# Optimization experiments

Hardware: AMD Instinct MI355X
Metric: run time of the kernel (lower is better)

The kernel has to match this reference:

```python
import jax, jax.numpy as jnp
import numpy as np

N_NODES = 1500
N_EDGES = 12000
IN_FEAT = 512
HIDDEN = 64
OUT_FEAT = 32
HEADS = 8
NEG_SLOPE = 0.2  # DGL GATConv default leaky_relu slope


def setup_inputs() -> dict:
    key = jax.random.key(0)
    ks = jax.random.split(key, 16)

    def xav(k, shape, fan_in):
        return jax.random.normal(k, shape, jnp.float32) * (1.0 / np.sqrt(fan_in))

    return {
        "node": jax.random.normal(ks[0], (N_NODES, IN_FEAT), jnp.float32),
        "src": jax.random.randint(ks[1], (N_EDGES,), 0, N_NODES, jnp.int32),
        "dst": jax.random.randint(ks[2], (N_EDGES,), 0, N_NODES, jnp.int32),
        "W1": xav(ks[3], (IN_FEAT, HEADS * HIDDEN), IN_FEAT),
        "al1": xav(ks[4], (HEADS, HIDDEN), HIDDEN),
        "ar1": xav(ks[5], (HEADS, HIDDEN), HIDDEN),
        "b1": jnp.zeros((HEADS, HIDDEN), jnp.float32),
        "W2": xav(ks[6], (HIDDEN, HEADS * HIDDEN), HIDDEN),
        "al2": xav(ks[7], (HEADS, HIDDEN), HIDDEN),
        "ar2": xav(ks[8], (HEADS, HIDDEN), HIDDEN),
        "b2": jnp.zeros((HEADS, HIDDEN), jnp.float32),
        "W3": xav(ks[9], (HIDDEN, HEADS * OUT_FEAT), HIDDEN),
        "al3": xav(ks[10], (HEADS, OUT_FEAT), OUT_FEAT),
        "ar3": xav(ks[11], (HEADS, OUT_FEAT), OUT_FEAT),
        "b3": jnp.zeros((HEADS, OUT_FEAT), jnp.float32),
    }


def gat_layer(h, W, al, ar, b, src, dst, n_nodes):
    """DGL GATConv semantics: h has shape [N, *prefix, F_in]; output [N, *prefix, H, F_out]."""
    H, Fo = al.shape
    feat = (h @ W).reshape(h.shape[:-1] + (H, Fo))          # [N, *P, H, Fo]
    el = (feat * al).sum(-1)                                 # [N, *P, H]
    er = (feat * ar).sum(-1)                                 # [N, *P, H]
    e = jax.nn.leaky_relu(el[src] + er[dst], NEG_SLOPE)      # [E, *P, H]
    # numerically stable edge softmax over incoming edges of each dst node
    emax = jax.lax.stop_gradient(jax.ops.segment_max(e, dst, num_segments=n_nodes))
    ex = jnp.exp(e - emax[dst])
    den = jax.ops.segment_sum(ex, dst, num_segments=n_nodes)
    a = ex / den[dst]                                        # [E, *P, H]
    msg = a[..., None] * feat[src]                           # [E, *P, H, Fo]
    return jax.ops.segment_sum(msg, dst, num_segments=n_nodes) + b


def reference(node, src, dst, W1, al1, ar1, b1, W2, al2, ar2, b2, W3, al3, ar3, b3):
    n = node.shape[0]
    h = gat_layer(node, W1, al1, ar1, b1, src, dst, n)       # [N, 8, 64]
    h = jax.nn.gelu(h, approximate=False)
    h = gat_layer(h, W2, al2, ar2, b2, src, dst, n)          # [N, 8, 8, 64]
    h = jax.nn.gelu(h, approximate=False)
    return gat_layer(h, W3, al3, ar3, b3, src, dst, n)       # [N, 8, 8, 8, 32]
```

## Files before the change

### kernel.cpp

```cpp
#include <hip/hip_runtime.h>
#include <math.h>

#define N_NODES 1500
#define N_EDGES 12000
#define IN_FEAT 512
#define HIDDEN 64
#define OUT_FEAT 32
#define HEADS 8

typedef short bf16x8 __attribute__((ext_vector_type(8)));
typedef float f32x4 __attribute__((ext_vector_type(4)));

__device__ __forceinline__ unsigned short f2bf(float f) {
    unsigned u = __float_as_uint(f);
    u += 0x7fff + ((u >> 16) & 1);
    return (unsigned short)(u >> 16);
}
__device__ __forceinline__ float bf2f(unsigned short b) {
    return __uint_as_float(((unsigned)b) << 16);
}
__device__ __forceinline__ unsigned packbf(float a) {
    unsigned short hi = f2bf(a);
    unsigned short lo = f2bf(a - bf2f(hi));
    return (unsigned)hi | ((unsigned)lo << 16);
}
__device__ __forceinline__ float rdlanef(float v, int c) {
    return __uint_as_float(__builtin_amdgcn_readlane(__float_as_uint(v), c));
}


__global__ void prep_kernel(const float* __restrict__ W2, const float* __restrict__ al2,
                            const float* __restrict__ ar2,
                            const float* __restrict__ W3, const float* __restrict__ al3,
                            const float* __restrict__ ar3,
                            float* __restrict__ aleff2, float* __restrict__ areff2,
                            float* __restrict__ aleff3, float* __restrict__ areff3,
                            float* __restrict__ W4t2,
                            unsigned* __restrict__ wfhi, unsigned* __restrict__ wflo,
                            int* __restrict__ counts, int* __restrict__ cursor) {
    int i = blockIdx.x * blockDim.x + threadIdx.x;
    if (i < 1536) {
        if (i < N_NODES + 1) counts[i] = 0;
        return;
    }
    i -= 1536;
    if (i < 1536) {
        if (i < N_NODES) cursor[i] = 0;
        return;
    }
    i -= 1536;
    if (i < 1024) {
        int lr = i >> 9; i &= 511;
        int h = i >> 6, k = i & 63;
        const float* a = lr ? ar2 : al2;
        float s = 0.f;
        for (int f = 0; f < 64; ++f)
            s = fmaf(W2[(size_t)k * 512 + h * 64 + f], a[h * 64 + f], s);
        (lr ? areff2 : aleff2)[h * 64 + k] = s;
        return;
    }
    i -= 1024;
    if (i < 1024) {
        int lr = i >> 9; i &= 511;
        int h = i >> 6, k = i & 63;
        const float* a = lr ? ar3 : al3;
        float s = 0.f;
        for (int f = 0; f < 32; ++f)
            s = fmaf(W3[(size_t)k * 256 + h * 32 + f], a[h * 32 + f], s);
        (lr ? areff3 : aleff3)[h * 64 + k] = s;
        return;
    }
    i -= 1024;
    if (i < 16 * 512 * 4) {
        int kg = i >> 11, rem = i & 2047;
        int c = rem >> 2, j = rem & 3;
        W4t2[i] = W2[(size_t)(kg * 4 + j) * 512 + c];
        return;
    }
    i -= 16 * 512 * 4;
    if (i < 16384) {
        int plane = i >> 13;
        int rem = i & 8191;
        int j2 = rem & 3, l = (rem >> 2) & 63;
        int ks = (rem >> 8) & 1, nt = (rem >> 9) & 1, h = (rem >> 10) & 7;
        int col = h * 32 + nt * 16 + (l & 15);
        int kb = ks * 32 + (l >> 4) * 8 + 2 * j2;
        unsigned parts[2];
        #pragma unroll
        for (int q = 0; q < 2; ++q) {
            float w = W3[(size_t)(kb + q) * 256 + col];
            unsigned short hi = f2bf(w);
            parts[q] = plane ? (unsigned)f2bf(w - bf2f(hi)) : (unsigned)hi;
        }
        unsigned word = parts[0] | (parts[1] << 16);
        (plane ? wflo : wfhi)[rem] = word;
    }
}

__global__ void hist_kernel(const int* __restrict__ dst, int* __restrict__ counts) {
    int e = blockIdx.x * blockDim.x + threadIdx.x;
    if (e < N_EDGES) atomicAdd(&counts[dst[e]], 1);
}

__global__ void scan_kernel(const int* __restrict__ counts, int* __restrict__ row_ptr) {
    __shared__ int part[256];
    int t = threadIdx.x;
    const int CH = (N_NODES + 255) / 256;
    int base = t * CH;
    int loc[8];
    int s = 0;
    for (int i = 0; i < CH; ++i) {
        int idx = base + i;
        int v = (idx < N_NODES) ? counts[idx] : 0;
        loc[i] = s;
        s += v;
    }
    part[t] = s;
    __syncthreads();
    if (t == 0) {
        int a = 0;
        for (int i = 0; i < 256; ++i) { int v = part[i]; part[i] = a; a += v; }
        row_ptr[N_NODES] = a;
    }
    __syncthreads();
    int p0 = part[t];
    for (int i = 0; i < CH; ++i) {
        int idx = base + i;
        if (idx < N_NODES) row_ptr[idx] = p0 + loc[i];
    }
}

__global__ void scatter_kernel(const int* __restrict__ dst, const int* __restrict__ row_ptr,
                               int* __restrict__ cursor, int* __restrict__ tmp_eid) {
    int e = blockIdx.x * blockDim.x + threadIdx.x;
    if (e < N_EDGES) {
        int d = dst[e];
        int pos = row_ptr[d] + atomicAdd(&cursor[d], 1);
        tmp_eid[pos] = e;
    }
}

__global__ void sort_csr_kernel(const int* __restrict__ row_ptr, const int* __restrict__ tmp_eid,
                                const int* __restrict__ src, int* __restrict__ csr_src) {
    int wid = (blockIdx.x * blockDim.x + threadIdx.x) >> 6;
    int lane = threadIdx.x & 63;
    if (wid >= N_NODES) return;
    int r0 = row_ptr[wid], deg = row_ptr[wid + 1] - r0;
    for (int base = 0; base < deg; base += 64) {
        int i = base + lane;
        int my = (i < deg) ? tmp_eid[r0 + i] : 0x7fffffff;
        int rank = 0;
        for (int b2 = 0; b2 < deg; b2 += 64) {
            int other = (b2 + lane < deg) ? tmp_eid[r0 + b2 + lane] : 0x7fffffff;
            int cnt2 = min(deg - b2, 64);
            for (int j = 0; j < cnt2; ++j) {
                int oj = __shfl(other, j);
                rank += (oj < my) ? 1 : 0;
            }
        }
        if (i < deg) csr_src[r0 + rank] = src[my];
    }
}


#define GM 32
#define GN 32
#define GK 32

__global__ __launch_bounds__(256) void gemm_f32(const float* __restrict__ A,
                                                const float* __restrict__ B,
                                                float* __restrict__ C,
                                                int M, int N, int K) {
    __shared__ float As[GK][GM + 2];
    __shared__ float Bs[GK][GN + 2];
    int t = threadIdx.x;
    int col0 = blockIdx.x * GN, row0 = blockIdx.y * GM;
    int tx = t & 15, ty = t >> 4;
    int am = t >> 3, ak = (t & 7) * 4;
    int bk = t >> 3, bn = (t & 7) * 4;
    float acc[2][2] = {};
    for (int k0 = 0; k0 < K; k0 += GK) {
        int gr = row0 + am;
        float4 av = (gr < M) ? *(const float4*)&A[(size_t)gr * K + k0 + ak]
                             : make_float4(0.f, 0.f, 0.f, 0.f);
        float4 bv = *(const float4*)&B[(size_t)(k0 + bk) * N + col0 + bn];
        __syncthreads();
        As[ak + 0][am] = av.x; As[ak + 1][am] = av.y;
        As[ak + 2][am] = av.z; As[ak + 3][am] = av.w;
        *(float4*)&Bs[bk][bn] = bv;
        __syncthreads();
        #pragma unroll
        for (int kk = 0; kk < GK; ++kk) {
            float2 a2 = *(const float2*)&As[kk][ty * 2];
            float2 b2 = *(const float2*)&Bs[kk][tx * 2];
            acc[0][0] = fmaf(a2.x, b2.x, acc[0][0]);
            acc[0][1] = fmaf(a2.x, b2.y, acc[0][1]);
            acc[1][0] = fmaf(a2.y, b2.x, acc[1][0]);
            acc[1][1] = fmaf(a2.y, b2.y, acc[1][1]);
        }
    }
    #pragma unroll
    for (int i = 0; i < 2; ++i) {
        int gr = row0 + ty * 2 + i;
        if (gr < M) {
            float2 v = make_float2(acc[i][0], acc[i][1]);
            *(float2*)&C[(size_t)gr * N + col0 + tx * 2] = v;
        }
    }
}


__global__ void elr_feat_kernel(const float* __restrict__ feat, const float* __restrict__ al,
                                const float* __restrict__ ar, float* __restrict__ el,
                                float* __restrict__ er, int RH) {
    int idx = blockIdx.x * blockDim.x + threadIdx.x;
    if (idx >= RH) return;
    int h = idx & (HEADS - 1);
    const float* fp = feat + (size_t)idx * HIDDEN;
    float sl = 0.f, sr = 0.f;
    for (int f = 0; f < HIDDEN; ++f) {
        float v = fp[f];
        sl = fmaf(v, al[h * HIDDEN + f], sl);
        sr = fmaf(v, ar[h * HIDDEN + f], sr);
    }
    el[idx] = sl;
    er[idx] = sr;
}

__global__ void elr_row_kernel(const float* __restrict__ X, const float* __restrict__ alv,
                               const float* __restrict__ arv, float* __restrict__ el,
                               float* __restrict__ er, int R) {
    int r = blockIdx.x * blockDim.x + threadIdx.x;
    if (r >= R) return;
    const float4* x4 = (const float4*)(X + (size_t)r * 64);
    float sl[8] = {}, sr[8] = {};
    for (int kg = 0; kg < 16; ++kg) {
        float4 xv = x4[kg];
        #pragma unroll
        for (int h = 0; h < 8; ++h) {
            float4 a = *(const float4*)&alv[h * 64 + kg * 4];
            float4 b = *(const float4*)&arv[h * 64 + kg * 4];
            sl[h] = fmaf(xv.x, a.x, fmaf(xv.y, a.y, fmaf(xv.z, a.z, fmaf(xv.w, a.w, sl[h]))));
            sr[h] = fmaf(xv.x, b.x, fmaf(xv.y, b.y, fmaf(xv.z, b.z, fmaf(xv.w, b.w, sr[h]))));
        }
    }
    float* elp = el + (size_t)r * 8;
    float* erp = er + (size_t)r * 8;
    #pragma unroll
    for (int h = 0; h < 8; ++h) { elp[h] = sl[h]; erp[h] = sr[h]; }
}

__device__ __forceinline__ float gelu_exact(float v) {
    return 0.5f * v * (1.0f + erff(v * 0.70710678118654752440f));
}

__global__ __launch_bounds__(256) void agg_l1(
    const float* __restrict__ feat, const float* __restrict__ el, const float* __restrict__ er,
    const float* __restrict__ bias, const int* __restrict__ row_ptr,
    const int* __restrict__ csr_src, float* __restrict__ out) {
    int n = blockIdx.x;
    int t = threadIdx.x, wv = t >> 6, lane = t & 63;
    int h0 = 2 * wv;
    int r0 = row_ptr[n], deg = row_ptr[n + 1] - r0;
    float2 erv = *(const float2*)&er[n * 8 + h0];
    float den0 = 0.f, den1 = 0.f, a0 = 0.f, a1 = 0.f;
    for (int c0 = 0; c0 < deg; c0 += 64) {
        int cnt = min(deg - c0, 64);
        int src_r = (lane < cnt) ? csr_src[r0 + c0 + lane] : 0;
        auto do_edge = [&](int s) {
            float2 elv = *(const float2*)&el[s * 8 + h0];
            float x0 = feat[((size_t)s * 8 + h0) * 64 + lane];
            float x1 = feat[((size_t)s * 8 + h0 + 1) * 64 + lane];
            float e0 = elv.x + erv.x; e0 = e0 > 0.f ? e0 : 0.2f * e0;
            float e1 = elv.y + erv.y; e1 = e1 > 0.f ? e1 : 0.2f * e1;
            float w0 = __expf(e0), w1 = __expf(e1);
            den0 += w0; den1 += w1;
            a0 = fmaf(w0, x0, a0);
            a1 = fmaf(w1, x1, a1);
        };
        int i = 0;
        for (; i + 2 <= cnt; i += 2) {
            int s0 = __builtin_amdgcn_readlane(src_r, i);
            int s1 = __builtin_amdgcn_readlane(src_r, i + 1);
            do_edge(s0);
            do_edge(s1);
        }
        if (i < cnt) do_edge(__builtin_amdgcn_readlane(src_r, i));
    }
    float i0 = deg ? 1.f / den0 : 0.f;
    float i1 = deg ? 1.f / den1 : 0.f;
    float v0 = a0 * i0 + bias[h0 * 64 + lane];
    float v1 = a1 * i1 + bias[(h0 + 1) * 64 + lane];
    out[((size_t)n * 8 + h0) * 64 + lane] = gelu_exact(v0);
    out[((size_t)n * 8 + h0 + 1) * 64 + lane] = gelu_exact(v1);
}

__global__ __launch_bounds__(256, 4) void agg_fused5(
    const float* __restrict__ X,
    const float* __restrict__ el, const float* __restrict__ er,
    const float* __restrict__ W4t,
    const float* __restrict__ bias,
    const int* __restrict__ row_ptr, const int* __restrict__ csr_src,
    float* __restrict__ out)
{
    constexpr int TOT = 512;
    constexpr int PTS = 68;
    constexpr int CHUNK = 64;

    int n = blockIdx.x;
    int r0 = row_ptr[n], deg = row_ptr[n + 1] - r0;
    int t = threadIdx.x, wv = t >> 6, lane = t & 63;

    __shared__ float inv_s[64];
    __shared__ float acc_s[8][8][68];
    __shared__ float wp_lds[64 * PTS];

    float agg0[8], agg1[8];
    #pragma unroll
    for (int h = 0; h < 8; ++h) { agg0[h] = 0.f; agg1[h] = 0.f; }
    float den = 0.f;

    int elbase_n = n * 8 * 8;
    int pA = wv * 2;
    float erv_t = er[elbase_n + lane];

    for (int c0 = 0; c0 < deg; c0 += CHUNK) {
        int cnt = min(deg - c0, CHUNK);
        int src_r = (lane < cnt) ? csr_src[r0 + c0 + lane] : 0;
        __syncthreads();
        for (int j = t; j < cnt * 64; j += 256) {
            int i = j >> 6;
            int s = __builtin_amdgcn_readlane(src_r, i);
            float e = el[(s * 8) * 8 + lane] + erv_t;
            e = e > 0.f ? e : 0.2f * e;
            wp_lds[i * 64 + lane] = __expf(e);
        }
        __syncthreads();
        if (t < 64) {
            for (int i = 0; i < cnt; ++i) den += wp_lds[i * 64 + t];
        }
        auto edge_fma = [&](int i) {
            int s = __builtin_amdgcn_readlane(src_r, i);
            const float* wp = &wp_lds[i * 64 + wv * 16];
            float4 w0 = *(const float4*)wp;
            float4 w1 = *(const float4*)(wp + 4);
            float4 w2 = *(const float4*)(wp + 8);
            float4 w3 = *(const float4*)(wp + 12);
            int xb = (s * 8 + pA) * 64 + lane;
            float xv0 = X[xb];
            float xv1 = X[xb + 64];
            agg0[0] = fmaf(w0.x, xv0, agg0[0]);
            agg0[1] = fmaf(w0.y, xv0, agg0[1]);
            agg0[2] = fmaf(w0.z, xv0, agg0[2]);
            agg0[3] = fmaf(w0.w, xv0, agg0[3]);
            agg0[4] = fmaf(w1.x, xv0, agg0[4]);
            agg0[5] = fmaf(w1.y, xv0, agg0[5]);
            agg0[6] = fmaf(w1.z, xv0, agg0[6]);
            agg0[7] = fmaf(w1.w, xv0, agg0[7]);
            agg1[0] = fmaf(w2.x, xv1, agg1[0]);
            agg1[1] = fmaf(w2.y, xv1, agg1[1]);
            agg1[2] = fmaf(w2.z, xv1, agg1[2]);
            agg1[3] = fmaf(w2.w, xv1, agg1[3]);
            agg1[4] = fmaf(w3.x, xv1, agg1[4]);
            agg1[5] = fmaf(w3.y, xv1, agg1[5]);
            agg1[6] = fmaf(w3.z, xv1, agg1[6]);
            agg1[7] = fmaf(w3.w, xv1, agg1[7]);
        };
        int i = 0;
        for (; i + 2 <= cnt; i += 2) { edge_fma(i); edge_fma(i + 1); }
        if (i < cnt) edge_fma(i);
    }
    if (t < 64) inv_s[t] = deg ? 1.f / den : 0.f;
    __syncthreads();
    {
        int pl0 = wv * 2;
        #pragma unroll
        for (int h = 0; h < 8; ++h) {
            acc_s[pl0][h][lane] = agg0[h] * inv_s[pl0 * 8 + h];
            acc_s[pl0 + 1][h][lane] = agg1[h] * inv_s[pl0 * 8 + 8 + h];
        }
    }
    __syncthreads();

    {
        int h = t >> 5, ft = t & 31;
        int f0 = ft * 2;
        float part[8][2];
        #pragma unroll
        for (int pl = 0; pl < 8; ++pl) { part[pl][0] = 0.f; part[pl][1] = 0.f; }
        #pragma unroll
        for (int kg = 0; kg < 16; ++kg) {
            float4 wr0 = *(const float4*)&W4t[(size_t)(kg * TOT + h * 64 + f0 + 0) * 4];
            float4 wr1 = *(const float4*)&W4t[(size_t)(kg * TOT + h * 64 + f0 + 1) * 4];
            #pragma unroll
            for (int pl = 0; pl < 8; ++pl) {
                float4 a4 = *(const float4*)&acc_s[pl][h][kg * 4];
                part[pl][0] = fmaf(a4.x, wr0.x, fmaf(a4.y, wr0.y,
                              fmaf(a4.z, wr0.z, fmaf(a4.w, wr0.w, part[pl][0]))));
                part[pl][1] = fmaf(a4.x, wr1.x, fmaf(a4.y, wr1.y,
                              fmaf(a4.z, wr1.z, fmaf(a4.w, wr1.w, part[pl][1]))));
            }
        }
        __syncthreads();
        #pragma unroll
        for (int pl = 0; pl < 8; ++pl)
            *(float2*)&wp_lds[(pl * 8 + h) * PTS + f0] = make_float2(part[pl][0], part[pl][1]);
    }
    __syncthreads();

    {
        for (int q = t; q < 1024; q += 256) {
            int pl = q >> 7, rem = q & 127;
            int h = rem >> 4, fq = rem & 15;
            int f0 = fq * 4;
            float4 acc4 = *(const float4*)&wp_lds[(pl * 8 + h) * PTS + f0];
            float4 b4 = *(const float4*)&bias[h * 64 + f0];
            acc4.x = gelu_exact(acc4.x + b4.x);
            acc4.y = gelu_exact(acc4.y + b4.y);
            acc4.z = gelu_exact(acc4.z + b4.z);
            acc4.w = gelu_exact(acc4.w + b4.w);
            *(float4*)&out[(size_t)(n * 8 + pl) * TOT + h * 64 + f0] = acc4;
        }
    }
}

__global__ __launch_bounds__(256, 8) void agg_mfma6(
    const float* __restrict__ X,
    const float* __restrict__ el, const float* __restrict__ er,
    const unsigned* __restrict__ wfhi, const unsigned* __restrict__ wflo,
    const float* __restrict__ bias,
    const int* __restrict__ row_ptr, const int* __restrict__ csr_src,
    float* __restrict__ out)
{
    int b = blockIdx.x;
    int n = b >> 2, pg = b & 3;
    int p0 = pg * 16;
    int r0 = row_ptr[n], deg = row_ptr[n + 1] - r0;
    int t = threadIdx.x, wv = t >> 6, lane = t & 63;
    int pA = p0 + wv * 4;

    __shared__ unsigned accH[4][16][68];

    int c = lane & 31;
    float erv = er[(n * 64 + pA) * 8 + c];

    float agg[4][8];
    #pragma unroll
    for (int q = 0; q < 4; ++q)
        #pragma unroll
        for (int h = 0; h < 8; ++h) agg[q][h] = 0.f;
    float den_half = 0.f;

    for (int c0 = 0; c0 < deg; c0 += 64) {
        int cnt = min(deg - c0, 64);
        int src_r = (lane < cnt) ? csr_src[r0 + c0 + lane] : 0;
        for (int it = 0; it < cnt; it += 4) {
            int i1 = min(it + 1, cnt - 1), i2 = min(it + 2, cnt - 1), i3 = min(it + 3, cnt - 1);
            int s0 = __builtin_amdgcn_readlane(src_r, it);
            int s1 = __builtin_amdgcn_readlane(src_r, i1);
            int s2 = __builtin_amdgcn_readlane(src_r, i2);
            int s3 = __builtin_amdgcn_readlane(src_r, i3);
            bool v1 = it + 1 < cnt, v2 = it + 2 < cnt, v3 = it + 3 < cnt;
            int sA = (lane < 32) ? s0 : s1;
            int sB = (lane < 32) ? s2 : s3;
            float eA = el[(sA * 64 + pA) * 8 + c] + erv;
            float eB = el[(sB * 64 + pA) * 8 + c] + erv;
            eA = eA > 0.f ? eA : 0.2f * eA;
            eB = eB > 0.f ? eB : 0.2f * eB;
            if (lane >= 32 && !v1) eA = -1e30f;
            if (lane < 32 && !v2) eB = -1e30f;
            if (lane >= 32 && !v3) eB = -1e30f;
            float wA = __expf(eA), wB = __expf(eB);
            den_half += wA + wB;
            int xb0 = (s0 * 64 + pA) * 64 + lane;
            int xb1 = (s1 * 64 + pA) * 64 + lane;
            int xb2 = (s2 * 64 + pA) * 64 + lane;
            int xb3 = (s3 * 64 + pA) * 64 + lane;
            float x0[4], x1[4], x2[4], x3[4];
            #pragma unroll
            for (int q = 0; q < 4; ++q) x0[q] = X[xb0 + q * 64];
            #pragma unroll
            for (int q = 0; q < 4; ++q) x1[q] = X[xb1 + q * 64];
            #pragma unroll
            for (int q = 0; q < 4; ++q) x2[q] = X[xb2 + q * 64];
            #pragma unroll
            for (int q = 0; q < 4; ++q) x3[q] = X[xb3 + q * 64];
            #pragma unroll
            for (int q = 0; q < 4; ++q) {
                #pragma unroll
                for (int h = 0; h < 8; ++h) {
                    agg[q][h] = fmaf(rdlanef(wA, q * 8 + h), x0[q], agg[q][h]);
                    agg[q][h] = fmaf(rdlanef(wA, 32 + q * 8 + h), x1[q], agg[q][h]);
                    agg[q][h] = fmaf(rdlanef(wB, q * 8 + h), x2[q], agg[q][h]);
                    agg[q][h] = fmaf(rdlanef(wB, 32 + q * 8 + h), x3[q], agg[q][h]);
                }
            }
        }
    }
    float den = den_half + __shfl(den_half, lane ^ 32);
    float inv = deg ? 1.f / den : 0.f;

    int m16 = lane & 15, g = lane >> 4;
    #pragma unroll
    for (int r = 0; r < 2; ++r) {
        if (r) __syncthreads();
        #pragma unroll
        for (int q = 0; q < 4; ++q) {
            int pl = wv * 4 + q;
            #pragma unroll
            for (int hh = 0; hh < 4; ++hh) {
                int h = 4 * r + hh;
                float iv = rdlanef(inv, q * 8 + h);
                accH[hh][pl][lane] = packbf(agg[q][h] * iv);
            }
        }
        __syncthreads();
        int h = 4 * r + wv;
        bf16x8 a_hi[2], a_lo[2];
        #pragma unroll
        for (int ks = 0; ks < 2; ++ks) {
            const unsigned* ap = &accH[wv][m16][ks * 32 + g * 8];
            uint4 q0 = *(const uint4*)ap;
            uint4 q1 = *(const uint4*)(ap + 4);
            a_hi[ks][0] = (short)(q0.x & 0xffffu); a_lo[ks][0] = (short)(q0.x >> 16);
            a_hi[ks][1] = (short)(q0.y & 0xffffu); a_lo[ks][1] = (short)(q0.y >> 16);
            a_hi[ks][2] = (short)(q0.z & 0xffffu); a_lo[ks][2] = (short)(q0.z >> 16);
            a_hi[ks][3] = (short)(q0.w & 0xffffu); a_lo[ks][3] = (short)(q0.w >> 16);
            a_hi[ks][4] = (short)(q1.x & 0xffffu); a_lo[ks][4] = (short)(q1.x >> 16);
            a_hi[ks][5] = (short)(q1.y & 0xffffu); a_lo[ks][5] = (short)(q1.y >> 16);
            a_hi[ks][6] = (short)(q1.z & 0xffffu); a_lo[ks][6] = (short)(q1.z >> 16);
            a_hi[ks][7] = (short)(q1.w & 0xffffu); a_lo[ks][7] = (short)(q1.w >> 16);
        }
        #pragma unroll
        for (int nt = 0; nt < 2; ++nt) {
            f32x4 D = {0.f, 0.f, 0.f, 0.f};
            #pragma unroll
            for (int ks = 0; ks < 2; ++ks) {
                size_t fb = (size_t)(((h * 2 + nt) * 2 + ks) * 64 + lane) * 4;
                bf16x8 b_hi = *(const bf16x8*)&wfhi[fb];
                bf16x8 b_lo = *(const bf16x8*)&wflo[fb];
                D = __builtin_amdgcn_mfma_f32_16x16x32_bf16(a_hi[ks], b_hi, D, 0, 0, 0);
                D = __builtin_amdgcn_mfma_f32_16x16x32_bf16(a_hi[ks], b_lo, D, 0, 0, 0);
                D = __builtin_amdgcn_mfma_f32_16x16x32_bf16(a_lo[ks], b_hi, D, 0, 0, 0);
            }
            float bv = bias[h * 32 + nt * 16 + m16];
            size_t ob = ((size_t)(n * 64) + p0 + g * 4) * 256 + h * 32 + nt * 16 + m16;
            out[ob]       = D[0] + bv;
            out[ob + 256] = D[1] + bv;
            out[ob + 512] = D[2] + bv;
            out[ob + 768] = D[3] + bv;
        }
    }
}


extern "C" void kernel_launch(void* const* d_in, const int* in_sizes, int n_in,
                              void* d_out, int out_size, void* d_ws, size_t ws_size,
                              hipStream_t stream) {
    const float* node = (const float*)d_in[0];
    const int* src = (const int*)d_in[1];
    const int* dst = (const int*)d_in[2];
    const float* W1 = (const float*)d_in[3];
    const float* al1 = (const float*)d_in[4];
    const float* ar1 = (const float*)d_in[5];
    const float* b1 = (const float*)d_in[6];
    const float* W2 = (const float*)d_in[7];
    const float* al2 = (const float*)d_in[8];
    const float* ar2 = (const float*)d_in[9];
    const float* b2 = (const float*)d_in[10];
    const float* W3 = (const float*)d_in[11];
    const float* al3 = (const float*)d_in[12];
    const float* ar3 = (const float*)d_in[13];
    const float* b3 = (const float*)d_in[14];
    float* out = (float*)d_out;

    char* ws = (char*)d_ws;
    size_t off = 0;
    auto alloc = [&](size_t nb) -> char* {
        char* q = ws + off;
        off += (nb + 255) & ~(size_t)255;
        return q;
    };
    int* counts   = (int*)alloc((N_NODES + 1) * sizeof(int));
    int* cursor   = (int*)alloc(N_NODES * sizeof(int));
    int* row_ptr  = (int*)alloc((N_NODES + 1) * sizeof(int));
    int* tmp_eid  = (int*)alloc(N_EDGES * sizeof(int));
    int* csr_src  = (int*)alloc(N_EDGES * sizeof(int));
    float* feat1  = (float*)alloc((size_t)N_NODES * 8 * 64 * 4);
    float* el1    = (float*)alloc((size_t)N_NODES * 8 * 4);
    float* er1    = (float*)alloc((size_t)N_NODES * 8 * 4);
    float* h1     = (float*)alloc((size_t)N_NODES * 8 * 64 * 4);
    float* aleff2 = (float*)alloc(8 * 64 * 4);
    float* areff2 = (float*)alloc(8 * 64 * 4);
    float* el2    = (float*)alloc((size_t)N_NODES * 8 * 8 * 4);
    float* er2    = (float*)alloc((size_t)N_NODES * 8 * 8 * 4);
    float* h2     = (float*)alloc((size_t)N_NODES * 64 * 64 * 4);
    float* aleff3 = (float*)alloc(8 * 64 * 4);
    float* areff3 = (float*)alloc(8 * 64 * 4);
    float* el3    = (float*)alloc((size_t)N_NODES * 64 * 8 * 4);
    float* er3    = (float*)alloc((size_t)N_NODES * 64 * 8 * 4);
    float* W4t2   = (float*)alloc((size_t)16 * 512 * 4 * 4);
    unsigned* wfhi = (unsigned*)alloc((size_t)8192 * 4);
    unsigned* wflo = (unsigned*)alloc((size_t)8192 * 4);

    const int PREP_T = 1536 + 1536 + 1024 + 1024 + 16 * 512 * 4 + 16384;
    prep_kernel<<<(PREP_T + 255) / 256, 256, 0, stream>>>(
        W2, al2, ar2, W3, al3, ar3, aleff2, areff2, aleff3, areff3, W4t2, wfhi, wflo,
        counts, cursor);

    hist_kernel<<<(N_EDGES + 255) / 256, 256, 0, stream>>>(dst, counts);
    scan_kernel<<<1, 256, 0, stream>>>(counts, row_ptr);
    scatter_kernel<<<(N_EDGES + 255) / 256, 256, 0, stream>>>(dst, row_ptr, cursor, tmp_eid);
    sort_csr_kernel<<<(N_NODES * 64 + 255) / 256, 256, 0, stream>>>(row_ptr, tmp_eid, src, csr_src);

    dim3 g1((512 + GN - 1) / GN, (N_NODES + GM - 1) / GM);
    gemm_f32<<<g1, 256, 0, stream>>>(node, W1, feat1, N_NODES, 512, IN_FEAT);
    elr_feat_kernel<<<(N_NODES * 8 + 255) / 256, 256, 0, stream>>>(feat1, al1, ar1, el1, er1, N_NODES * 8);
    agg_l1<<<N_NODES, 256, 0, stream>>>(feat1, el1, er1, b1, row_ptr, csr_src, h1);

    elr_row_kernel<<<(N_NODES * 8 + 255) / 256, 256, 0, stream>>>(h1, aleff2, areff2, el2, er2, N_NODES * 8);
    agg_fused5<<<N_NODES, 256, 0, stream>>>(h1, el2, er2, W4t2, b2, row_ptr, csr_src, h2);

    elr_row_kernel<<<(N_NODES * 64 + 255) / 256, 256, 0, stream>>>(h2, aleff3, areff3, el3, er3, N_NODES * 64);
    agg_mfma6<<<N_NODES * 4, 256, 0, stream>>>(h2, el3, er3, wfhi, wflo, b3, row_ptr, csr_src, out);
}
```

Before: 165.4 us.

## Fuse CSR build into one block, fold layer-3 el/er into agg_fused5

Replaces the four CSR construction kernels (hist, scan, scatter, sort) with a single 1024-thread block that does everything in LDS, which cuts launch overhead and global atomics at the cost of running serially on one CU. It also computes layer-3 el/er inside agg_fused5's epilogue with shuffle reductions, dropping the separate elr_row_kernel pass over h2. Separately, the final output stores become nontemporal and agg_mfma6's occupancy hint drops from 8 to 6 waves per SIMD.

After: 231.6 us. 1.4x slower.

```diff
diff --git a/kernel.cpp b/kernel.cpp
--- a/kernel.cpp
+++ b/kernel.cpp
@@ -36,19 +36,8 @@
                             float* __restrict__ aleff2, float* __restrict__ areff2,
                             float* __restrict__ aleff3, float* __restrict__ areff3,
                             float* __restrict__ W4t2,
-                            unsigned* __restrict__ wfhi, unsigned* __restrict__ wflo,
-                            int* __restrict__ counts, int* __restrict__ cursor) {
+                            unsigned* __restrict__ wfhi, unsigned* __restrict__ wflo) {
     int i = blockIdx.x * blockDim.x + threadIdx.x;
-    if (i < 1536) {
-        if (i < N_NODES + 1) counts[i] = 0;
-        return;
-    }
-    i -= 1536;
-    if (i < 1536) {
-        if (i < N_NODES) cursor[i] = 0;
-        return;
-    }
-    i -= 1536;
     if (i < 1024) {
         int lr = i >> 9; i &= 511;
         int h = i >> 6, k = i & 63;
@@ -97,68 +86,54 @@
     }
 }
 
-__global__ void hist_kernel(const int* __restrict__ dst, int* __restrict__ counts) {
-    int e = blockIdx.x * blockDim.x + threadIdx.x;
-    if (e < N_EDGES) atomicAdd(&counts[dst[e]], 1);
-}
-
-__global__ void scan_kernel(const int* __restrict__ counts, int* __restrict__ row_ptr) {
-    __shared__ int part[256];
+__global__ __launch_bounds__(1024) void csr_build_kernel(
+    const int* __restrict__ dst, const int* __restrict__ src,
+    int* __restrict__ row_ptr, int* __restrict__ csr_src) {
+    __shared__ int cnt[N_NODES + 1];
+    __shared__ int rp[N_NODES + 1];
+    __shared__ int eid[N_EDGES];
+    __shared__ int part[1024];
     int t = threadIdx.x;
-    const int CH = (N_NODES + 255) / 256;
-    int base = t * CH;
-    int loc[8];
-    int s = 0;
-    for (int i = 0; i < CH; ++i) {
-        int idx = base + i;
-        int v = (idx < N_NODES) ? counts[idx] : 0;
-        loc[i] = s;
-        s += v;
-    }
-    part[t] = s;
+    for (int i = t; i <= N_NODES; i += 1024) cnt[i] = 0;
+    __syncthreads();
+    for (int e = t; e < N_EDGES; e += 1024) atomicAdd(&cnt[dst[e]], 1);
+    __syncthreads();
+    int base = t * 2;
+    int v0 = (base < N_NODES) ? cnt[base] : 0;
+    int v1 = (base + 1 < N_NODES) ? cnt[base + 1] : 0;
+    part[t] = v0 + v1;
     __syncthreads();
     if (t == 0) {
         int a = 0;
-        for (int i = 0; i < 256; ++i) { int v = part[i]; part[i] = a; a += v; }
-        row_ptr[N_NODES] = a;
-    }
-    __syncthreads();
-    int p0 = part[t];
-    for (int i = 0; i < CH; ++i) {
-        int idx = base + i;
-        if (idx < N_NODES) row_ptr[idx] = p0 + loc[i];
-    }
-}
-
-__global__ void scatter_kernel(const int* __restrict__ dst, const int* __restrict__ row_ptr,
-                               int* __restrict__ cursor, int* __restrict__ tmp_eid) {
-    int e = blockIdx.x * blockDim.x + threadIdx.x;
-    if (e < N_EDGES) {
+        for (int i = 0; i < 1024; ++i) { int v = part[i]; part[i] = a; a += v; }
+        rp[N_NODES] = a;
+    }
+    __syncthreads();
+    if (base < N_NODES) rp[base] = part[t];
+    if (base + 1 < N_NODES) rp[base + 1] = part[t] + v0;
+    __syncthreads();
+    for (int i = t; i <= N_NODES; i += 1024) row_ptr[i] = rp[i];
+    for (int i = t; i <= N_NODES; i += 1024) cnt[i] = 0;
+    __syncthreads();
+    for (int e = t; e < N_EDGES; e += 1024) {
         int d = dst[e];
-        int pos = row_ptr[d] + atomicAdd(&cursor[d], 1);
-        tmp_eid[pos] = e;
-    }
-}
-
-__global__ void sort_csr_kernel(const int* __restrict__ row_ptr, const int* __restrict__ tmp_eid,
-                                const int* __restrict__ src, int* __restrict__ csr_src) {
-    int wid = (blockIdx.x * blockDim.x + threadIdx.x) >> 6;
-    int lane = threadIdx.x & 63;
-    if (wid >= N_NODES) return;
-    int r0 = row_ptr[wid], deg = row_ptr[wid + 1] - r0;
-    for (int base = 0; base < deg; base += 64) {
-        int i = base + lane;
-        int my = (i < deg) ? tmp_eid[r0 + i] : 0x7fffffff;
-        int rank = 0;
-        for (int b2 = 0; b2 < deg; b2 += 64) {
-            int other = (b2 + lane < deg) ? tmp_eid[r0 + b2 + lane] : 0x7fffffff;
-            int cnt2 = min(deg - b2, 64);
-            for (int j = 0; j < cnt2; ++j) {
-                int oj = __shfl(other, j);
+        int pos = rp[d] + atomicAdd(&cnt[d], 1);
+        eid[pos] = e;
+    }
+    __syncthreads();
+    int wv = t >> 6, lane = t & 63;
+    for (int nd = wv; nd < N_NODES; nd += 16) {
+        int r0 = rp[nd], deg = rp[nd + 1] - r0;
+        for (int b0 = 0; b0 < deg; b0 += 64) {
+            int i = b0 + lane;
+            int my = (i < deg) ? eid[r0 + i] : 0x7fffffff;
+            int rank = 0;
+            for (int j = 0; j < deg; ++j) {
+                int oj = eid[r0 + j];
                 rank += (oj < my) ? 1 : 0;
             }
-        }
-        if (i < deg) csr_src[r0 + rank] = src[my];
+            if (i < deg) csr_src[r0 + rank] = src[my];
+        }
     }
 }
 
@@ -300,8 +275,10 @@
     const float* __restrict__ el, const float* __restrict__ er,
     const float* __restrict__ W4t,
     const float* __restrict__ bias,
+    const float* __restrict__ alv3, const float* __restrict__ arv3,
     const int* __restrict__ row_ptr, const int* __restrict__ csr_src,
-    float* __restrict__ out)
+    float* __restrict__ out,
+    float* __restrict__ el3, float* __restrict__ er3)
 {
     constexpr int TOT = 512;
     constexpr int PTS = 68;
@@ -409,10 +386,12 @@
     __syncthreads();
 
     {
-        for (int q = t; q < 1024; q += 256) {
-            int pl = q >> 7, rem = q & 127;
-            int h = rem >> 4, fq = rem & 15;
-            int f0 = fq * 4;
+        int rem = t & 127;
+        int h = rem >> 4, fq = rem & 15;
+        int f0 = fq * 4;
+        #pragma unroll
+        for (int it = 0; it < 4; ++it) {
+            int pl = (t >> 7) + 2 * it;
             float4 acc4 = *(const float4*)&wp_lds[(pl * 8 + h) * PTS + f0];
             float4 b4 = *(const float4*)&bias[h * 64 + f0];
             acc4.x = gelu_exact(acc4.x + b4.x);
@@ -420,11 +399,32 @@
             acc4.z = gelu_exact(acc4.z + b4.z);
             acc4.w = gelu_exact(acc4.w + b4.w);
             *(float4*)&out[(size_t)(n * 8 + pl) * TOT + h * 64 + f0] = acc4;
-        }
-    }
-}
-
-__global__ __launch_bounds__(256, 8) void agg_mfma6(
+            float sel = 0.f;
+            #pragma unroll
+            for (int j = 0; j < 8; ++j) {
+                float4 a4 = *(const float4*)&alv3[j * 64 + f0];
+                float4 r4 = *(const float4*)&arv3[j * 64 + f0];
+                float pe = fmaf(acc4.x, a4.x, fmaf(acc4.y, a4.y,
+                           fmaf(acc4.z, a4.z, acc4.w * a4.w)));
+                float pr = fmaf(acc4.x, r4.x, fmaf(acc4.y, r4.y,
+                           fmaf(acc4.z, r4.z, acc4.w * r4.w)));
+                #pragma unroll
+                for (int m = 1; m < 16; m <<= 1) {
+                    pe += __shfl_xor(pe, m);
+                    pr += __shfl_xor(pr, m);
+                }
+                sel = (fq == j) ? pe : sel;
+                sel = (fq == 8 + j) ? pr : sel;
+            }
+            int p = pl * 8 + h;
+            size_t rbase = ((size_t)n * 64 + p) * 8;
+            float* dstp = (fq < 8) ? &el3[rbase + fq] : &er3[rbase + (fq - 8)];
+            *dstp = sel;
+        }
+    }
+}
+
+__global__ __launch_bounds__(256, 6) void agg_mfma6(
     const float* __restrict__ X,
     const float* __restrict__ el, const float* __restrict__ er,
     const unsigned* __restrict__ wfhi, const unsigned* __restrict__ wflo,
@@ -545,10 +545,10 @@
             }
             float bv = bias[h * 32 + nt * 16 + m16];
             size_t ob = ((size_t)(n * 64) + p0 + g * 4) * 256 + h * 32 + nt * 16 + m16;
-            out[ob]       = D[0] + bv;
-            out[ob + 256] = D[1] + bv;
-            out[ob + 512] = D[2] + bv;
-            out[ob + 768] = D[3] + bv;
+            __builtin_nontemporal_store(D[0] + bv, &out[ob]);
+            __builtin_nontemporal_store(D[1] + bv, &out[ob + 256]);
+            __builtin_nontemporal_store(D[2] + bv, &out[ob + 512]);
+            __builtin_nontemporal_store(D[3] + bv, &out[ob + 768]);
         }
     }
 }
@@ -581,10 +581,7 @@
         off += (nb + 255) & ~(size_t)255;
         return q;
     };
-    int* counts   = (int*)alloc((N_NODES + 1) * sizeof(int));
-    int* cursor   = (int*)alloc(N_NODES * sizeof(int));
     int* row_ptr  = (int*)alloc((N_NODES + 1) * sizeof(int));
-    int* tmp_eid  = (int*)alloc(N_EDGES * sizeof(int));
     int* csr_src  = (int*)alloc(N_EDGES * sizeof(int));
     float* feat1  = (float*)alloc((size_t)N_NODES * 8 * 64 * 4);
     float* el1    = (float*)alloc((size_t)N_NODES * 8 * 4);
@@ -603,15 +600,11 @@
     unsigned* wfhi = (unsigned*)alloc((size_t)8192 * 4);
     unsigned* wflo = (unsigned*)alloc((size_t)8192 * 4);
 
-    const int PREP_T = 1536 + 1536 + 1024 + 1024 + 16 * 512 * 4 + 16384;
+    const int PREP_T = 1024 + 1024 + 16 * 512 * 4 + 16384;
     prep_kernel<<<(PREP_T + 255) / 256, 256, 0, stream>>>(
-        W2, al2, ar2, W3, al3, ar3, aleff2, areff2, aleff3, areff3, W4t2, wfhi, wflo,
-        counts, cursor);
-
-    hist_kernel<<<(N_EDGES + 255) / 256, 256, 0, stream>>>(dst, counts);
-    scan_kernel<<<1, 256, 0, stream>>>(counts, row_ptr);
-    scatter_kernel<<<(N_EDGES + 255) / 256, 256, 0, stream>>>(dst, row_ptr, cursor, tmp_eid);
-    sort_csr_kernel<<<(N_NODES * 64 + 255) / 256, 256, 0, stream>>>(row_ptr, tmp_eid, src, csr_src);
+        W2, al2, ar2, W3, al3, ar3, aleff2, areff2, aleff3, areff3, W4t2, wfhi, wflo);
+
+    csr_build_kernel<<<1, 1024, 0, stream>>>(dst, src, row_ptr, csr_src);
 
     dim3 g1((512 + GN - 1) / GN, (N_NODES + GM - 1) / GM);
     gemm_f32<<<g1, 256, 0, stream>>>(node, W1, feat1, N_NODES, 512, IN_FEAT);
@@ -619,8 +612,8 @@
     agg_l1<<<N_NODES, 256, 0, stream>>>(feat1, el1, er1, b1, row_ptr, csr_src, h1);
 
     elr_row_kernel<<<(N_NODES * 8 + 255) / 256, 256, 0, stream>>>(h1, aleff2, areff2, el2, er2, N_NODES * 8);
-    agg_fused5<<<N_NODES, 256, 0, stream>>>(h1, el2, er2, W4t2, b2, row_ptr, csr_src, h2);
-
-    elr_row_kernel<<<(N_NODES * 64 + 255) / 256, 256, 0, stream>>>(h2, aleff3, areff3, el3, er3, N_NODES * 64);
+    agg_fused5<<<N_NODES, 256, 0, stream>>>(h1, el2, er2, W4t2, b2, aleff3, areff3,
+                                            row_ptr, csr_src, h2, el3, er3);
+
     agg_mfma6<<<N_NODES * 4, 256, 0, stream>>>(h2, el3, er3, wfhi, wflo, b3, row_ptr, csr_src, out);
 }
```
